# Kernel tuning notes

Measured on AMD Instinct MI355X. Metric: run time of the kernel, lower is better.

Reference implementation:

```python
import jax, jax.numpy as jnp
import numpy as np

EPS = 1e-5
SLOPE = 0.2
K = 20
BINS = [1, 2, 4, 8, 16, 32]


def knn(x_t, k):
    # x_t: (B, N, C) -> idx (B, N, k) of nearest neighbors (by L2, incl. self)
    xx = jnp.sum(x_t * x_t, axis=-1)  # (B, N)
    pd = 2.0 * jnp.einsum('bnc,bmc->bnm', x_t, x_t) - xx[:, :, None] - xx[:, None, :]
    _, idx = jax.lax.top_k(pd, k)
    return idx


def edge_features(x_t, idx):
    # x_t: (B, N, C), idx: (B, N, k) -> (B, N, k, 2C) = [nbr - ctr, ctr]
    B = x_t.shape[0]
    nbr = x_t[jnp.arange(B)[:, None, None], idx]          # (B, N, k, C) gather
    ctr = jnp.broadcast_to(x_t[:, :, None, :], nbr.shape)
    return jnp.concatenate([nbr - ctr, ctr], axis=-1)


def batchnorm(h, gamma, beta, axes):
    # training-mode BN: normalize with batch statistics over `axes` (channel last)
    m = jnp.mean(h, axis=axes, keepdims=True)
    v = jnp.var(h, axis=axes, keepdims=True)
    return (h - m) * jax.lax.rsqrt(v + EPS) * gamma + beta


def lrelu(h):
    return jnp.where(h >= 0, h, SLOPE * h)


def edgeconv(x_t, W, g, b):
    # 1x1 conv over edge features + BN + LeakyReLU + max over k neighbors
    e = edge_features(x_t, knn(x_t, K))            # (B, N, k, 2C)
    h = jnp.einsum('bnkc,oc->bnko', e, W)          # per-edge GEMM
    h = lrelu(batchnorm(h, g, b, (0, 1, 2)))
    return jnp.max(h, axis=2)                      # (B, N, Cout)


def setup_inputs() -> dict:
    key = jax.random.key(0)
    ks = jax.random.split(key, 8)
    B, N = 4, 2048
    d = {'x': jax.random.normal(ks[0], (B, 3, N), dtype=jnp.float32)}
    # conv weights (out, in); BN gamma=1, beta=0 as in torch init
    d['W1'] = jax.random.normal(ks[1], (64, 6), dtype=jnp.float32) * 0.1
    d['g1'] = jnp.ones((64,), jnp.float32); d['b1'] = jnp.zeros((64,), jnp.float32)
    d['W2'] = jax.random.normal(ks[2], (64, 128), dtype=jnp.float32) * 0.1
    d['g2'] = jnp.ones((64,), jnp.float32); d['b2'] = jnp.zeros((64,), jnp.float32)
    d['W3'] = jax.random.normal(ks[3], (128, 128), dtype=jnp.float32) * 0.1
    d['g3'] = jnp.ones((128,), jnp.float32); d['b3'] = jnp.zeros((128,), jnp.float32)
    d['W4'] = jax.random.normal(ks[4], (256, 256), dtype=jnp.float32) * 0.1
    d['g4'] = jnp.ones((256,), jnp.float32); d['b4'] = jnp.zeros((256,), jnp.float32)
    d['W5'] = jax.random.normal(ks[5], (1024, 512), dtype=jnp.float32) * 0.05
    d['g5'] = jnp.ones((1024,), jnp.float32); d['b5'] = jnp.zeros((1024,), jnp.float32)
    d['Wf'] = jax.random.normal(ks[6], (256, 1024), dtype=jnp.float32) * 0.03
    d['bfeat'] = jax.random.normal(ks[7], (256,), dtype=jnp.float32) * 0.01
    return d


def reference(x, W1, g1, b1, W2, g2, b2, W3, g3, b3, W4, g4, b4, W5, g5, b5, Wf, bfeat):
    B, _, N = x.shape
    x_t = jnp.transpose(x, (0, 2, 1))              # (B, N, 3)
    x1 = edgeconv(x_t, W1, g1, b1)                 # (B, N, 64)
    x2 = edgeconv(x1, W2, g2, b2)                  # (B, N, 64)
    x3 = edgeconv(x2, W3, g3, b3)                  # (B, N, 128)
    x4 = edgeconv(x3, W4, g4, b4)                  # (B, N, 256)
    xc = jnp.concatenate([x1, x2, x3, x4], axis=-1)  # (B, N, 512)
    h = jnp.einsum('bnc,oc->bno', xc, W5)          # (B, N, 1024)
    h = lrelu(batchnorm(h, g5, b5, (0, 1)))
    F = h.shape[-1]
    feats = []
    for nb in BINS:  # horizontal pyramid pooling over contiguous point chunks
        z = h.reshape(B, nb, N // nb, F)
        feats.append(jnp.max(z, axis=2) + jnp.mean(z, axis=2))
    bins = jnp.concatenate(feats, axis=1)          # (B, 63, F)
    out = jnp.einsum('bsf,of->sbo', bins, Wf) + bfeat  # (63, B, 256)
    return out
```

## Files before the change

kernel.cpp:

```cpp
#include <hip/hip_runtime.h>
#include <hip/hip_bf16.h>
#include <cstdint>
#include <cstddef>

#define B_SZ   4
#define N_PTS  2048
#define KNN    20
#define BN_ROWS (B_SZ * N_PTS)
#define EPSV   1e-5f
#define SLOPEV 0.2f

#define MODE_GD   0
#define MODE_DIST 1

typedef __attribute__((ext_vector_type(8))) short bf16x8;
typedef __attribute__((ext_vector_type(4))) float f32x4;

__global__ void k_transpose(const float* __restrict__ x, float* __restrict__ xt,
                            float* __restrict__ xx)
{
    int i = blockIdx.x * 256 + threadIdx.x;
    if (i >= BN_ROWS) return;
    int b = i >> 11, n = i & 2047;
    float v0 = x[((b * 3 + 0) << 11) + n];
    float v1 = x[((b * 3 + 1) << 11) + n];
    float v2 = x[((b * 3 + 2) << 11) + n];
    xt[i * 3 + 0] = v0; xt[i * 3 + 1] = v1; xt[i * 3 + 2] = v2;
    xx[i] = fmaf(v0, v0, fmaf(v1, v1, v2 * v2));
}

__global__ void k_prepw_all(const float* __restrict__ W1, const float* __restrict__ W2,
                            const float* __restrict__ W3, const float* __restrict__ W4,
                            const float* __restrict__ W5, const float* __restrict__ Wf,
                            float* __restrict__ wc, __hip_bfloat16* __restrict__ w5h,
                            float* __restrict__ wft)
{
    int i = blockIdx.x * 256 + threadIdx.x;
    if (i >= 876928) return;
    if (i >= 614784) {
        int e = i - 614784;
        int o = e >> 10, f = e & 1023;
        wft[f * 256 + o] = Wf[e];
        return;
    }
    if (i >= 90496) {
        int e = i - 90496;
        w5h[e] = __float2bfloat16(W5[e]);
        return;
    }
    const float* W; int O, C, off;
    if      (i < 384)   { W = W1; O = 64;  C = 3;   off = 0; }
    else if (i < 8576)  { W = W2; O = 64;  C = 64;  off = 384; }
    else if (i < 24960) { W = W3; O = 128; C = 64;  off = 8576; }
    else                { W = W4; O = 256; C = 128; off = 24960; }
    int e = i - off, j = e / C, c = e - j * C;
    float v;
    if (j < O) v = W[j * 2 * C + c];
    else { int jo = j - O; v = W[jo * 2 * C + C + c] - W[jo * 2 * C + c]; }
    wc[i] = v;
}

template<int MODE, bool VEC>
__launch_bounds__(256)
__global__ void k_mm128(const float* __restrict__ A, int lda,
                        const float* __restrict__ Bm, int ldb,
                        const float* __restrict__ xx, int b0,
                        float* __restrict__ C1, float* __restrict__ C2,
                        int Nn, int Kd)
{
    constexpr int LDA_ = 132;
    constexpr int LDB_ = (MODE == MODE_DIST) ? 132 : 68;
    constexpr int SMEMF = 32 * LDA_ + 32 * LDB_;
    __shared__ float smem[SMEMF];
    float* As = smem;
    float* Bs = smem + 32 * LDA_;
    float* T  = smem;
    const int tid = threadIdx.x;
    const int tx  = tid & 15;
    const int ty  = tid >> 4;

    int m0, n0;
    if constexpr (MODE == MODE_DIST) {
        int t = blockIdx.x;
        int it, jt;
        if (t < 120) {
            int i = 0;
            for (; i < 15; ++i) { int cnt = 15 - i; if (t < cnt) break; t -= cnt; }
            it = i; jt = i + 1 + t;
        } else {
            it = jt = t - 120;
        }
        m0 = it * 128;
        n0 = jt * 128;
    } else {
        m0 = blockIdx.y * 128;
        n0 = blockIdx.x * 64;
    }

    const float* Ab;
    const float* Bb;
    int ldbe;
    if constexpr (MODE == MODE_DIST) {
        const int b = b0 + blockIdx.z;
        Ab = A + (size_t)b * N_PTS * lda;
        Bb = Ab;
        ldbe = lda;
    } else {
        Ab = A; Bb = Bm; ldbe = ldb;
    }

    constexpr int NJH = (MODE == MODE_DIST) ? 2 : 1;
    float acc[2][NJH][4][4] = {};

    for (int k0 = 0; k0 < Kd; k0 += 32) {
        #pragma unroll
        for (int r = 0; r < 4; ++r) {
            int e = r * 256 + tid, row = e >> 3, kq = e & 7;
            if constexpr (VEC) {
                float4 v = *(const float4*)&Ab[(size_t)(m0 + row) * lda + k0 + kq * 4];
                As[(kq * 4 + 0) * LDA_ + row] = v.x;
                As[(kq * 4 + 1) * LDA_ + row] = v.y;
                As[(kq * 4 + 2) * LDA_ + row] = v.z;
                As[(kq * 4 + 3) * LDA_ + row] = v.w;
            } else {
                #pragma unroll
                for (int j = 0; j < 4; ++j) {
                    int kg = k0 + kq * 4 + j;
                    As[(kq * 4 + j) * LDA_ + row] =
                        (kg < Kd) ? Ab[(size_t)(m0 + row) * lda + kg] : 0.f;
                }
            }
        }
        constexpr int BR = (MODE == MODE_DIST) ? 4 : 2;
        #pragma unroll
        for (int r = 0; r < BR; ++r) {
            int e = r * 256 + tid, row = e >> 3, kq = e & 7;
            if constexpr (VEC) {
                float4 v = *(const float4*)&Bb[(size_t)(n0 + row) * ldbe + k0 + kq * 4];
                Bs[(kq * 4 + 0) * LDB_ + row] = v.x;
                Bs[(kq * 4 + 1) * LDB_ + row] = v.y;
                Bs[(kq * 4 + 2) * LDB_ + row] = v.z;
                Bs[(kq * 4 + 3) * LDB_ + row] = v.w;
            } else {
                #pragma unroll
                for (int j = 0; j < 4; ++j) {
                    int kg = k0 + kq * 4 + j;
                    Bs[(kq * 4 + j) * LDB_ + row] =
                        (kg < Kd) ? Bb[(size_t)(n0 + row) * ldbe + kg] : 0.f;
                }
            }
        }
        __syncthreads();

        int klen = Kd - k0; if (klen > 32) klen = 32;
        #pragma unroll 8
        for (int kk = 0; kk < klen; ++kk) {
            float4 a0 = *(const float4*)&As[kk * LDA_ + ty * 4];
            float4 a1 = *(const float4*)&As[kk * LDA_ + 64 + ty * 4];
            float av[2][4] = {{a0.x,a0.y,a0.z,a0.w},{a1.x,a1.y,a1.z,a1.w}};
            if constexpr (MODE == MODE_DIST) {
                float4 b0q = *(const float4*)&Bs[kk * LDB_ + tx * 4];
                float4 b1q = *(const float4*)&Bs[kk * LDB_ + 64 + tx * 4];
                float bw[2][4] = {{b0q.x,b0q.y,b0q.z,b0q.w},{b1q.x,b1q.y,b1q.z,b1q.w}};
                #pragma unroll
                for (int ih = 0; ih < 2; ++ih)
                    #pragma unroll
                    for (int jh = 0; jh < 2; ++jh)
                        #pragma unroll
                        for (int ii = 0; ii < 4; ++ii)
                            #pragma unroll
                            for (int jj = 0; jj < 4; ++jj)
                                acc[ih][jh][ii][jj] = fmaf(av[ih][ii], bw[jh][jj], acc[ih][jh][ii][jj]);
            } else {
                float4 bq = *(const float4*)&Bs[kk * LDB_ + tx * 4];
                float bw[4] = {bq.x, bq.y, bq.z, bq.w};
                #pragma unroll
                for (int ih = 0; ih < 2; ++ih)
                    #pragma unroll
                    for (int ii = 0; ii < 4; ++ii)
                        #pragma unroll
                        for (int jj = 0; jj < 4; ++jj)
                            acc[ih][0][ii][jj] = fmaf(av[ih][ii], bw[jj], acc[ih][0][ii][jj]);
            }
        }
        __syncthreads();
    }

    if constexpr (MODE == MODE_DIST) {
        const float* xxb = xx + (b0 + blockIdx.z) * N_PTS;
        float xj[2][4];
        #pragma unroll
        for (int jh = 0; jh < 2; ++jh) {
            float4 v = *(const float4*)&xxb[n0 + jh * 64 + tx * 4];
            xj[jh][0] = v.x; xj[jh][1] = v.y; xj[jh][2] = v.z; xj[jh][3] = v.w;
        }
        float xiv[2][4];
        #pragma unroll
        for (int ih = 0; ih < 2; ++ih)
            #pragma unroll
            for (int i = 0; i < 4; ++i)
                xiv[ih][i] = xxb[m0 + ih * 64 + ty * 4 + i];
        const bool diag = (m0 == n0);
        const size_t zoff = (size_t)blockIdx.z * N_PTS;

        #pragma unroll
        for (int ih = 0; ih < 2; ++ih)
            #pragma unroll
            for (int i = 0; i < 4; ++i) {
                int gi = m0 + ih * 64 + ty * 4 + i;
                float xi = xiv[ih][i];
                size_t base = (zoff + gi) * N_PTS;
                #pragma unroll
                for (int jh = 0; jh < 2; ++jh) {
                    int gj = n0 + jh * 64 + tx * 4;
                    float4 v;
                    v.x = 2.f * acc[ih][jh][i][0] - xi - xj[jh][0];
                    v.y = 2.f * acc[ih][jh][i][1] - xi - xj[jh][1];
                    v.z = 2.f * acc[ih][jh][i][2] - xi - xj[jh][2];
                    v.w = 2.f * acc[ih][jh][i][3] - xi - xj[jh][3];
                    if (diag) {
                        if (gi == gj + 0) v.x = 0.f;
                        if (gi == gj + 1) v.y = 0.f;
                        if (gi == gj + 2) v.z = 0.f;
                        if (gi == gj + 3) v.w = 0.f;
                    }
                    *(float4*)&C1[base + gj] = v;
                }
            }

        if (!diag) {
            #pragma unroll
            for (int jh = 0; jh < 2; ++jh) {
                #pragma unroll
                for (int c = 0; c < 4; ++c) {
                    float xjc = xj[jh][c];
                    #pragma unroll
                    for (int ih = 0; ih < 2; ++ih) {
                        float4 tv;
                        tv.x = 2.f * acc[ih][jh][0][c] - xjc - xiv[ih][0];
                        tv.y = 2.f * acc[ih][jh][1][c] - xjc - xiv[ih][1];
                        tv.z = 2.f * acc[ih][jh][2][c] - xjc - xiv[ih][2];
                        tv.w = 2.f * acc[ih][jh][3][c] - xjc - xiv[ih][3];
                        *(float4*)&T[(tx * 4 + c) * LDA_ + ih * 64 + ty * 4] = tv;
                    }
                }
                __syncthreads();
                #pragma unroll
                for (int r = 0; r < 8; ++r) {
                    int e = r * 256 + tid;
                    int jr = e >> 5, c4 = e & 31;
                    float4 tv = *(const float4*)&T[jr * LDA_ + c4 * 4];
                    *(float4*)&C1[(zoff + n0 + jh * 64 + jr) * N_PTS + m0 + c4 * 4] = tv;
                }
                __syncthreads();
            }
        }
    } else {
        const int Oo = Nn >> 1;
        #pragma unroll
        for (int ih = 0; ih < 2; ++ih)
            #pragma unroll
            for (int i = 0; i < 4; ++i) {
                int row = m0 + ih * 64 + ty * 4 + i;
                int colg = n0 + tx * 4;
                float4 v = make_float4(acc[ih][0][i][0], acc[ih][0][i][1],
                                       acc[ih][0][i][2], acc[ih][0][i][3]);
                if (colg < Oo) *(float4*)&C1[(size_t)row * Oo + colg] = v;
                else           *(float4*)&C2[(size_t)row * Oo + colg - Oo] = v;
            }
    }
}

__launch_bounds__(256)
__global__ void k_gemm5(const unsigned short* __restrict__ Ah,
                        const unsigned short* __restrict__ Bh,
                        float* __restrict__ Cf,
                        float* __restrict__ ssum, float* __restrict__ ssumsq)
{
    constexpr int LDA = 72;
    __shared__ unsigned short As[128 * LDA];
    __shared__ unsigned short Bs[128 * LDA];
    const int tid  = threadIdx.x;
    const int lane = tid & 63;
    const int w    = tid >> 6;
    const int wr   = w >> 1, wcl = w & 1;
    const int quad = lane >> 4;
    const int l16  = lane & 15;
    const int m0 = blockIdx.y * 128;
    const int n0 = blockIdx.x * 128;

    f32x4 acc[4][4] = {};

    for (int k0 = 0; k0 < 512; k0 += 64) {
        #pragma unroll
        for (int r = 0; r < 4; ++r) {
            int e = r * 256 + tid, row = e >> 3, kq = e & 7;
            *(uint4*)&As[row * LDA + kq * 8] =
                *(const uint4*)&Ah[(size_t)(m0 + row) * 512 + k0 + kq * 8];
        }
        #pragma unroll
        for (int r = 0; r < 4; ++r) {
            int e = r * 256 + tid, row = e >> 3, kq = e & 7;
            *(uint4*)&Bs[row * LDA + kq * 8] =
                *(const uint4*)&Bh[(size_t)(n0 + row) * 512 + k0 + kq * 8];
        }
        __syncthreads();
        #pragma unroll
        for (int kk = 0; kk < 64; kk += 32) {
            bf16x8 af[4], bfr[4];
            #pragma unroll
            for (int i = 0; i < 4; ++i)
                af[i] = *(const bf16x8*)&As[(wr * 64 + i * 16 + l16) * LDA + kk + quad * 8];
            #pragma unroll
            for (int j = 0; j < 4; ++j)
                bfr[j] = *(const bf16x8*)&Bs[(wcl * 64 + j * 16 + l16) * LDA + kk + quad * 8];
            #pragma unroll
            for (int i = 0; i < 4; ++i)
                #pragma unroll
                for (int j = 0; j < 4; ++j)
                    acc[i][j] = __builtin_amdgcn_mfma_f32_16x16x32_bf16(af[i], bfr[j], acc[i][j], 0, 0, 0);
        }
        __syncthreads();
    }

    #pragma unroll
    for (int i = 0; i < 4; ++i) {
        int rbase = m0 + wr * 64 + i * 16 + quad * 4;
        #pragma unroll
        for (int j = 0; j < 4; ++j) {
            int col = n0 + wcl * 64 + j * 16 + l16;
            #pragma unroll
            for (int r = 0; r < 4; ++r)
                Cf[(size_t)(rbase + r) * 1024 + col] = acc[i][j][r];
        }
    }

    float* sredS = (float*)As;
    float* sredQ = (float*)Bs;
    #pragma unroll
    for (int j = 0; j < 4; ++j) {
        float s = 0.f, q = 0.f;
        #pragma unroll
        for (int i = 0; i < 4; ++i)
            #pragma unroll
            for (int r = 0; r < 4; ++r) {
                float v = acc[i][j][r];
                s += v; q = fmaf(v, v, q);
            }
        int coll = wcl * 64 + j * 16 + l16;
        int slot = wr * 4 + quad;
        sredS[coll * 8 + slot] = s;
        sredQ[coll * 8 + slot] = q;
    }
    __syncthreads();
    if (tid < 128) {
        float s = 0.f, q = 0.f;
        #pragma unroll
        for (int t = 0; t < 8; ++t) { s += sredS[tid * 8 + t]; q += sredQ[tid * 8 + t]; }
        ssum  [blockIdx.y * 1024 + n0 + tid] = s;
        ssumsq[blockIdx.y * 1024 + n0 + tid] = q;
    }
}

__launch_bounds__(256)
__global__ void k_select(const float* __restrict__ D2, int* __restrict__ idx_out)
{
    const int lane = threadIdx.x & 63;
    const int w    = threadIdx.x >> 6;
    const int qloc = blockIdx.x * 4 + w;
    const float* row = D2 + (size_t)qloc * N_PTS;

    unsigned key[32];
    #pragma unroll
    for (int c = 0; c < 8; ++c) {
        float4 v = *(const float4*)&row[c * 256 + lane * 4];
        float vv[4] = {v.x, v.y, v.z, v.w};
        #pragma unroll
        for (int r = 0; r < 4; ++r) {
            unsigned u = __float_as_uint(vv[r]);
            key[c * 4 + r] = ((int)u >= 0) ? (u | 0x80000000u) : ~u;
        }
    }

    unsigned lo = 0u, hi = 0xFFFFFFFFu;
    while (lo < hi) {
        unsigned mid = lo + ((hi - lo) >> 1);
        int cnt = 0;
        #pragma unroll
        for (int e = 0; e < 32; ++e)
            cnt += __popcll(__ballot(key[e] > mid));
        if (cnt < KNN) hi = mid; else lo = mid + 1;
    }
    const unsigned T = lo;

    int* outp = idx_out + (size_t)qloc * KNN;
    const unsigned long long ltmask = (lane == 0) ? 0ull : (~0ull >> (64 - lane));
    int base = 0;
    #pragma unroll
    for (int e = 0; e < 32; ++e) {
        bool p = key[e] > T;
        unsigned long long m = __ballot(p);
        if (p) {
            int pos = base + __popcll(m & ltmask);
            outp[pos] = (e >> 2) * 256 + lane * 4 + (e & 3);
        }
        base += __popcll(m);
    }
    #pragma unroll
    for (int e = 0; e < 32; ++e) {
        bool p = key[e] == T;
        unsigned long long m = __ballot(p);
        if (p) {
            int pos = base + __popcll(m & ltmask);
            if (pos < KNN) outp[pos] = (e >> 2) * 256 + lane * 4 + (e & 3);
        }
        base += __popcll(m);
    }
}

template<int O, int NSEQ>
__launch_bounds__(256)
__global__ void k_gather(const float* __restrict__ gtab, const float* __restrict__ dtab,
                         const int* __restrict__ idx,
                         float* __restrict__ hmax, float* __restrict__ hmin,
                         float* __restrict__ ssum, float* __restrict__ ssumsq)
{
    constexpr int NPB = 256 / O;
    const int grp = threadIdx.x / O;
    const int o   = threadIdx.x & (O - 1);
    float accS = 0.f, accS2 = 0.f;
    const int rowsPerBlock = NPB * NSEQ;
    const int batch = blockIdx.x & 3;
    const int chunk = blockIdx.x >> 2;
    const int bbase = batch << 11;
    for (int s = 0; s < NSEQ; ++s) {
        int row = bbase + chunk * rowsPerBlock + s * NPB + grp;
        const int* ip = idx + (size_t)row * KNN;
        float gmax = -INFINITY, gmin = INFINITY, gs = 0.f, gs2 = 0.f;
        for (int k = 0; k < KNN; ++k) {
            int nb = ip[k];
            float v = gtab[(size_t)(bbase + nb) * O + o];
            gmax = fmaxf(gmax, v);
            gmin = fminf(gmin, v);
            gs  += v;
            gs2  = fmaf(v, v, gs2);
        }
        float d = dtab[(size_t)row * O + o];
        hmax[(size_t)row * O + o] = gmax + d;
        hmin[(size_t)row * O + o] = gmin + d;
        accS  += gs + (float)KNN * d;
        accS2 += gs2 + 2.f * d * gs + (float)KNN * d * d;
    }
    int bank = blockIdx.x & 63;
    atomicAdd(&ssum[bank * O + o], accS);
    atomicAdd(&ssumsq[bank * O + o], accS2);
}

template<int O, bool WRITE_XX>
__launch_bounds__(256)
__global__ void k_normalize(const float* __restrict__ hmax, const float* __restrict__ hmin,
                            const float* __restrict__ ssum, const float* __restrict__ ssumsq,
                            const float* __restrict__ gamma, const float* __restrict__ beta,
                            float invM, float* __restrict__ xcs,
                            __hip_bfloat16* __restrict__ xch, float* __restrict__ xx)
{
    const int tid = threadIdx.x;
    const int o   = tid & (O - 1);
    float s = 0.f, s2 = 0.f;
    #pragma unroll 8
    for (int bk = 0; bk < 64; ++bk) { s += ssum[bk * O + o]; s2 += ssumsq[bk * O + o]; }
    float mean = s * invM;
    float var  = fmaf(-mean, mean, s2 * invM);
    float sc   = gamma[o] * rsqrtf(var + EPSV);
    float sh   = beta[o] - mean * sc;

    constexpr int R = 256 / O;
    const int rloc = tid / O;
    __shared__ float part[4];
    const int ngroups = BN_ROWS / R;
    for (int gidx = blockIdx.x; gidx < ngroups; gidx += gridDim.x) {
        int row = gidx * R + rloc;
        size_t i = (size_t)row * O + o;
        float h = (sc >= 0.f) ? hmax[i] : hmin[i];
        float y = fmaf(h, sc, sh);
        y = (y >= 0.f) ? y : SLOPEV * y;
        xcs[(size_t)row * 512 + o] = y;
        xch[(size_t)row * 512 + o] = __float2bfloat16(y);
        if constexpr (WRITE_XX) {
            float p = y * y;
            #pragma unroll
            for (int sft = 32; sft >= 1; sft >>= 1) p += __shfl_xor(p, sft, 64);
            if constexpr (O == 64) {
                if ((tid & 63) == 0) xx[row] = p;
            } else {
                if ((tid & 63) == 0) part[tid >> 6] = p;
                __syncthreads();
                if constexpr (O == 128) {
                    if (tid < 2) xx[gidx * R + tid] = part[2 * tid] + part[2 * tid + 1];
                } else {
                    if (tid == 0) xx[gidx * R] = (part[0] + part[1]) + (part[2] + part[3]);
                }
                __syncthreads();
            }
        }
    }
}

__global__ void k_seg(const float* __restrict__ h,
                      const float* __restrict__ ssum, const float* __restrict__ ssumsq,
                      const float* __restrict__ gamma, const float* __restrict__ beta,
                      float* __restrict__ smax, float* __restrict__ ssumseg)
{
    int f = blockIdx.y * 256 + threadIdx.x;
    float s = 0.f, s2 = 0.f;
    #pragma unroll 8
    for (int bk = 0; bk < 64; ++bk) { s += ssum[bk * 1024 + f]; s2 += ssumsq[bk * 1024 + f]; }
    const float invM = 1.f / (float)BN_ROWS;
    float mean = s * invM;
    float var  = fmaf(-mean, mean, s2 * invM);
    float sc   = gamma[f] * rsqrtf(var + EPSV);
    float sh   = beta[f] - mean * sc;

    int seg = blockIdx.x;
    float mx = -INFINITY, sm = 0.f;
    int n0 = seg * 64;
    for (int i = 0; i < 64; ++i) {
        float v = fmaf(h[(size_t)(n0 + i) * 1024 + f], sc, sh);
        v = (v >= 0.f) ? v : SLOPEV * v;
        mx = fmaxf(mx, v); sm += v;
    }
    smax[(size_t)seg * 1024 + f]    = mx;
    ssumseg[(size_t)seg * 1024 + f] = sm;
}

__launch_bounds__(256)
__global__ void k_final(const float* __restrict__ smax, const float* __restrict__ ssg,
                        const float* __restrict__ Wft, const float* __restrict__ bfeat,
                        float* __restrict__ out)
{
    __shared__ float row[1024];
    __shared__ float part[1024];
    const int tid = threadIdx.x;
    int sb = blockIdx.x;
    int s = sb >> 2, b = sb & 3;
    int nb = (s == 0) ? 1 : (s < 3) ? 2 : (s < 7) ? 4 : (s < 15) ? 8 : (s < 31) ? 16 : 32;
    int idxL = s - (nb - 1);
    int segc = 32 / nb;
    int seg0 = b * 32 + idxL * segc;
    float inv = 1.f / (float)(64 * segc);
    for (int c = tid; c < 1024; c += 256) {
        float mx = -INFINITY, sm = 0.f;
        for (int t = 0; t < segc; ++t) {
            mx = fmaxf(mx, smax[(size_t)(seg0 + t) * 1024 + c]);
            sm += ssg[(size_t)(seg0 + t) * 1024 + c];
        }
        row[c] = mx + sm * inv;
    }
    __syncthreads();

    const int lane = tid & 63;
    const int w    = tid >> 6;
    const float* rw = row + w * 256;
    const float* wp = Wft + (size_t)(w * 256) * 256 + lane * 4;
    float4 a0 = {0,0,0,0}, a1 = {0,0,0,0}, a2 = {0,0,0,0}, a3 = {0,0,0,0};
    for (int f = 0; f < 256; f += 4) {
        float r0 = rw[f + 0], r1 = rw[f + 1], r2 = rw[f + 2], r3 = rw[f + 3];
        float4 w0 = *(const float4*)&wp[(size_t)(f + 0) * 256];
        float4 w1 = *(const float4*)&wp[(size_t)(f + 1) * 256];
        float4 w2 = *(const float4*)&wp[(size_t)(f + 2) * 256];
        float4 w3 = *(const float4*)&wp[(size_t)(f + 3) * 256];
        a0.x = fmaf(r0, w0.x, a0.x); a0.y = fmaf(r0, w0.y, a0.y);
        a0.z = fmaf(r0, w0.z, a0.z); a0.w = fmaf(r0, w0.w, a0.w);
        a1.x = fmaf(r1, w1.x, a1.x); a1.y = fmaf(r1, w1.y, a1.y);
        a1.z = fmaf(r1, w1.z, a1.z); a1.w = fmaf(r1, w1.w, a1.w);
        a2.x = fmaf(r2, w2.x, a2.x); a2.y = fmaf(r2, w2.y, a2.y);
        a2.z = fmaf(r2, w2.z, a2.z); a2.w = fmaf(r2, w2.w, a2.w);
        a3.x = fmaf(r3, w3.x, a3.x); a3.y = fmaf(r3, w3.y, a3.y);
        a3.z = fmaf(r3, w3.z, a3.z); a3.w = fmaf(r3, w3.w, a3.w);
    }
    float4 a;
    a.x = (a0.x + a1.x) + (a2.x + a3.x);
    a.y = (a0.y + a1.y) + (a2.y + a3.y);
    a.z = (a0.z + a1.z) + (a2.z + a3.z);
    a.w = (a0.w + a1.w) + (a2.w + a3.w);
    *(float4*)&part[w * 256 + lane * 4] = a;
    __syncthreads();
    int o = tid;
    float acc = (part[o] + part[256 + o]) + (part[512 + o] + part[768 + o]);
    out[(size_t)sb * 256 + o] = acc + bfeat[o];
}

extern "C" void kernel_launch(void* const* d_in, const int* in_sizes, int n_in,
                              void* d_out, int out_size, void* d_ws, size_t ws_size,
                              hipStream_t stream)
{
    const float* x  = (const float*)d_in[0];
    const float* W1 = (const float*)d_in[1];
    const float* g1 = (const float*)d_in[2];
    const float* b1 = (const float*)d_in[3];
    const float* W2 = (const float*)d_in[4];
    const float* g2 = (const float*)d_in[5];
    const float* b2 = (const float*)d_in[6];
    const float* W3 = (const float*)d_in[7];
    const float* g3 = (const float*)d_in[8];
    const float* b3 = (const float*)d_in[9];
    const float* W4 = (const float*)d_in[10];
    const float* g4 = (const float*)d_in[11];
    const float* b4 = (const float*)d_in[12];
    const float* W5 = (const float*)d_in[13];
    const float* g5 = (const float*)d_in[14];
    const float* b5 = (const float*)d_in[15];
    const float* Wf = (const float*)d_in[16];
    const float* bfeat = (const float*)d_in[17];
    float* out = (float*)d_out;
    float* ws  = (float*)d_ws;

    float* xt1   = ws + 0;
    int*   idx   = (int*)(ws + 24576);
    float* xx    = ws + 188416;
    float* xc    = ws + 196608;
    float* hmax  = ws + 4390912;
    float* hmin  = ws + 6488064;
    float* stats = ws + 8585216;
    float* smax  = ws + 8650752;
    float* ssg   = ws + 8781824;
    float* wc    = ws + 8912896;
    float* big   = ws + 9003520;
    float* gtab  = big;
    float* dtab  = big + 2097152;
    __hip_bfloat16* xch = (__hip_bfloat16*)(ws + 25780736);
    __hip_bfloat16* w5h = (__hip_bfloat16*)(ws + 27877888);
    float* wft   = ws + 28140032;
    float* l5s   = ws + 28402176;
    float* l5q   = ws + 28467712;

    hipMemsetAsync(stats, 0, 65536 * sizeof(float), stream);
    k_transpose<<<32, 256, 0, stream>>>(x, xt1, xx);
    k_prepw_all<<<3426, 256, 0, stream>>>(W1, W2, W3, W4, W5, Wf, wc, w5h, wft);

    const float invMk = 1.f / (float)(BN_ROWS * KNN);

    {
        float* ss = stats + 0;
        k_mm128<MODE_DIST, false><<<dim3(136, 1, 4), 256, 0, stream>>>(xt1, 3, nullptr, 0, xx, 0, big, nullptr, N_PTS, 3);
        k_select<<<2048, 256, 0, stream>>>(big, idx);
        k_mm128<MODE_GD, false><<<dim3(2, 64, 1), 256, 0, stream>>>(xt1, 3, wc, 3, nullptr, 0, gtab, dtab, 128, 3);
        k_gather<64, 8><<<256, 256, 0, stream>>>(gtab, dtab, idx, hmax, hmin, ss, ss + 4096);
        k_normalize<64, true><<<512, 256, 0, stream>>>(hmax, hmin, ss, ss + 4096, g1, b1, invMk, xc + 0, xch + 0, xx);
    }
    {
        float* ss = stats + 8192;
        k_mm128<MODE_DIST, true><<<dim3(136, 1, 4), 256, 0, stream>>>(xc + 0, 512, nullptr, 0, xx, 0, big, nullptr, N_PTS, 64);
        k_select<<<2048, 256, 0, stream>>>(big, idx);
        k_mm128<MODE_GD, true><<<dim3(2, 64, 1), 256, 0, stream>>>(xc + 0, 512, wc + 384, 64, nullptr, 0, gtab, dtab, 128, 64);
        k_gather<64, 8><<<256, 256, 0, stream>>>(gtab, dtab, idx, hmax, hmin, ss, ss + 4096);
        k_normalize<64, true><<<512, 256, 0, stream>>>(hmax, hmin, ss, ss + 4096, g2, b2, invMk, xc + 64, xch + 64, xx);
    }
    {
        float* ss = stats + 16384;
        k_mm128<MODE_DIST, true><<<dim3(136, 1, 4), 256, 0, stream>>>(xc + 64, 512, nullptr, 0, xx, 0, big, nullptr, N_PTS, 64);
        k_select<<<2048, 256, 0, stream>>>(big, idx);
        k_mm128<MODE_GD, true><<<dim3(4, 64, 1), 256, 0, stream>>>(xc + 64, 512, wc + 8576, 64, nullptr, 0, gtab, dtab, 256, 64);
        k_gather<128, 8><<<512, 256, 0, stream>>>(gtab, dtab, idx, hmax, hmin, ss, ss + 8192);
        k_normalize<128, true><<<512, 256, 0, stream>>>(hmax, hmin, ss, ss + 8192, g3, b3, invMk, xc + 128, xch + 128, xx);
    }
    {
        float* ss = stats + 32768;
        k_mm128<MODE_DIST, true><<<dim3(136, 1, 4), 256, 0, stream>>>(xc + 128, 512, nullptr, 0, xx, 0, big, nullptr, N_PTS, 128);
        k_select<<<2048, 256, 0, stream>>>(big, idx);
        k_mm128<MODE_GD, true><<<dim3(8, 64, 1), 256, 0, stream>>>(xc + 128, 512, wc + 24960, 128, nullptr, 0, gtab, dtab, 512, 128);
        k_gather<256, 8><<<1024, 256, 0, stream>>>(gtab, dtab, idx, hmax, hmin, ss, ss + 16384);
        k_normalize<256, false><<<512, 256, 0, stream>>>(hmax, hmin, ss, ss + 16384, g4, b4, invMk, xc + 256, xch + 256, xx);
    }
    {
        k_gemm5<<<dim3(8, 64), 256, 0, stream>>>((const unsigned short*)xch, (const unsigned short*)w5h, big, l5s, l5q);
        k_seg<<<dim3(128, 4), 256, 0, stream>>>(big, l5s, l5q, g5, b5, smax, ssg);
        k_final<<<252, 256, 0, stream>>>(smax, ssg, wft, bfeat, out);
    }
}
```

Measured before the change: 577.1 us.

## Split distance GEMM tiles into 128x64 items with atomic work-queue scheduling

Replaces the 256-thread 128x128 pairwise-distance tile kernel with a 128-thread 128x64 variant. Tiles are claimed through an atomic ticket counter instead of blockIdx, giving 1088 smaller work items that balance better across CUs. The symmetric mirror write is restructured per 64-column half. The GD weight GEMM path also moves to 128 threads. The cost is smaller blocks with lower per-thread reuse, plus an extra atomic and barrier per tile.

Result: slower. 700.7 us (+21.4%).

```diff
diff --git a/kernel.cpp b/kernel.cpp
--- a/kernel.cpp
+++ b/kernel.cpp
@@ -61,107 +61,105 @@
 }
 
 template<int MODE, bool VEC>
-__launch_bounds__(256)
-__global__ void k_mm128(const float* __restrict__ A, int lda,
-                        const float* __restrict__ Bm, int ldb,
-                        const float* __restrict__ xx, int b0,
-                        float* __restrict__ C1, float* __restrict__ C2,
-                        int Nn, int Kd)
+__launch_bounds__(128)
+__global__ void k_mm64(const float* __restrict__ A, int lda,
+                       const float* __restrict__ Bm, int ldb,
+                       const float* __restrict__ xx, int* __restrict__ tick,
+                       float* __restrict__ C1, float* __restrict__ C2,
+                       int Nn, int Kd)
 {
     constexpr int LDA_ = 132;
-    constexpr int LDB_ = (MODE == MODE_DIST) ? 132 : 68;
-    constexpr int SMEMF = 32 * LDA_ + 32 * LDB_;
-    __shared__ float smem[SMEMF];
+    constexpr int LDB_ = 68;
+    __shared__ float smem[32 * LDA_ + 32 * LDB_];
+    __shared__ int s_t;
     float* As = smem;
     float* Bs = smem + 32 * LDA_;
     float* T  = smem;
     const int tid = threadIdx.x;
-    const int tx  = tid & 15;
-    const int ty  = tid >> 4;
-
-    int m0, n0;
-    if constexpr (MODE == MODE_DIST) {
-        int t = blockIdx.x;
-        int it, jt;
-        if (t < 120) {
-            int i = 0;
-            for (; i < 15; ++i) { int cnt = 15 - i; if (t < cnt) break; t -= cnt; }
-            it = i; jt = i + 1 + t;
+    const int tx  = tid & 7;
+    const int ty  = tid >> 3;
+
+    for (;;) {
+        int m0, n0, bz = 0;
+        bool diagitem = false, mirror = false;
+        if constexpr (MODE == MODE_DIST) {
+            if (tid == 0) s_t = atomicAdd(tick, 1);
+            __syncthreads();
+            const int t = s_t;
+            if (t >= 1088) return;
+            bz = t & 3;
+            int u = t >> 2;
+            int it, jt, half;
+            if (u < 240) {
+                int p = u >> 1; half = u & 1; mirror = true;
+                int i = 0;
+                for (; i < 15; ++i) { int cnt = 15 - i; if (p < cnt) break; p -= cnt; }
+                it = i; jt = i + 1 + p;
+            } else {
+                int d = u - 240; it = jt = d >> 1; half = d & 1; diagitem = true;
+            }
+            m0 = it * 128;
+            n0 = jt * 128 + half * 64;
         } else {
-            it = jt = t - 120;
-        }
-        m0 = it * 128;
-        n0 = jt * 128;
-    } else {
-        m0 = blockIdx.y * 128;
-        n0 = blockIdx.x * 64;
-    }
-
-    const float* Ab;
-    const float* Bb;
-    int ldbe;
-    if constexpr (MODE == MODE_DIST) {
-        const int b = b0 + blockIdx.z;
-        Ab = A + (size_t)b * N_PTS * lda;
-        Bb = Ab;
-        ldbe = lda;
-    } else {
-        Ab = A; Bb = Bm; ldbe = ldb;
-    }
-
-    constexpr int NJH = (MODE == MODE_DIST) ? 2 : 1;
-    float acc[2][NJH][4][4] = {};
-
-    for (int k0 = 0; k0 < Kd; k0 += 32) {
-        #pragma unroll
-        for (int r = 0; r < 4; ++r) {
-            int e = r * 256 + tid, row = e >> 3, kq = e & 7;
-            if constexpr (VEC) {
-                float4 v = *(const float4*)&Ab[(size_t)(m0 + row) * lda + k0 + kq * 4];
-                As[(kq * 4 + 0) * LDA_ + row] = v.x;
-                As[(kq * 4 + 1) * LDA_ + row] = v.y;
-                As[(kq * 4 + 2) * LDA_ + row] = v.z;
-                As[(kq * 4 + 3) * LDA_ + row] = v.w;
-            } else {
-                #pragma unroll
-                for (int j = 0; j < 4; ++j) {
-                    int kg = k0 + kq * 4 + j;
-                    As[(kq * 4 + j) * LDA_ + row] =
-                        (kg < Kd) ? Ab[(size_t)(m0 + row) * lda + kg] : 0.f;
+            m0 = blockIdx.y * 128;
+            n0 = blockIdx.x * 64;
+        }
+
+        const float* Ab; const float* Bb; int ldbe;
+        if constexpr (MODE == MODE_DIST) {
+            Ab = A + (size_t)bz * N_PTS * lda;  Bb = Ab;  ldbe = lda;
+        } else { Ab = A; Bb = Bm; ldbe = ldb; }
+
+        float acc[2][2][4][4] = {};
+
+        for (int k0 = 0; k0 < Kd; k0 += 32) {
+            #pragma unroll
+            for (int r = 0; r < 8; ++r) {
+                int e = r * 128 + tid, row = e >> 3, kq = e & 7;
+                if constexpr (VEC) {
+                    float4 v = *(const float4*)&Ab[(size_t)(m0 + row) * lda + k0 + kq * 4];
+                    As[(kq * 4 + 0) * LDA_ + row] = v.x;
+                    As[(kq * 4 + 1) * LDA_ + row] = v.y;
+                    As[(kq * 4 + 2) * LDA_ + row] = v.z;
+                    As[(kq * 4 + 3) * LDA_ + row] = v.w;
+                } else {
+                    #pragma unroll
+                    for (int j = 0; j < 4; ++j) {
+                        int kg = k0 + kq * 4 + j;
+                        As[(kq * 4 + j) * LDA_ + row] =
+                            (kg < Kd) ? Ab[(size_t)(m0 + row) * lda + kg] : 0.f;
+                    }
                 }
             }
-        }
-        constexpr int BR = (MODE == MODE_DIST) ? 4 : 2;
-        #pragma unroll
-        for (int r = 0; r < BR; ++r) {
-            int e = r * 256 + tid, row = e >> 3, kq = e & 7;
-            if constexpr (VEC) {
-                float4 v = *(const float4*)&Bb[(size_t)(n0 + row) * ldbe + k0 + kq * 4];
-                Bs[(kq * 4 + 0) * LDB_ + row] = v.x;
-                Bs[(kq * 4 + 1) * LDB_ + row] = v.y;
-                Bs[(kq * 4 + 2) * LDB_ + row] = v.z;
-                Bs[(kq * 4 + 3) * LDB_ + row] = v.w;
-            } else {
-                #pragma unroll
-                for (int j = 0; j < 4; ++j) {
-                    int kg = k0 + kq * 4 + j;
-                    Bs[(kq * 4 + j) * LDB_ + row] =
-                        (kg < Kd) ? Bb[(size_t)(n0 + row) * ldbe + kg] : 0.f;
+            #pragma unroll
+            for (int r = 0; r < 4; ++r) {
+                int e = r * 128 + tid, row = e >> 3, kq = e & 7;
+                if constexpr (VEC) {
+                    float4 v = *(const float4*)&Bb[(size_t)(n0 + row) * ldbe + k0 + kq * 4];
+                    Bs[(kq * 4 + 0) * LDB_ + row] = v.x;
+                    Bs[(kq * 4 + 1) * LDB_ + row] = v.y;
+                    Bs[(kq * 4 + 2) * LDB_ + row] = v.z;
+                    Bs[(kq * 4 + 3) * LDB_ + row] = v.w;
+                } else {
+                    #pragma unroll
+                    for (int j = 0; j < 4; ++j) {
+                        int kg = k0 + kq * 4 + j;
+                        Bs[(kq * 4 + j) * LDB_ + row] =
+                            (kg < Kd) ? Bb[(size_t)(n0 + row) * ldbe + kg] : 0.f;
+                    }
                 }
             }
-        }
-        __syncthreads();
-
-        int klen = Kd - k0; if (klen > 32) klen = 32;
-        #pragma unroll 8
-        for (int kk = 0; kk < klen; ++kk) {
-            float4 a0 = *(const float4*)&As[kk * LDA_ + ty * 4];
-            float4 a1 = *(const float4*)&As[kk * LDA_ + 64 + ty * 4];
-            float av[2][4] = {{a0.x,a0.y,a0.z,a0.w},{a1.x,a1.y,a1.z,a1.w}};
-            if constexpr (MODE == MODE_DIST) {
-                float4 b0q = *(const float4*)&Bs[kk * LDB_ + tx * 4];
-                float4 b1q = *(const float4*)&Bs[kk * LDB_ + 64 + tx * 4];
-                float bw[2][4] = {{b0q.x,b0q.y,b0q.z,b0q.w},{b1q.x,b1q.y,b1q.z,b1q.w}};
+            __syncthreads();
+
+            int klen = Kd - k0; if (klen > 32) klen = 32;
+            #pragma unroll 8
+            for (int kk = 0; kk < klen; ++kk) {
+                float4 a0 = *(const float4*)&As[kk * LDA_ + ty * 4];
+                float4 a1 = *(const float4*)&As[kk * LDA_ + 64 + ty * 4];
+                float4 b0 = *(const float4*)&Bs[kk * LDB_ + tx * 4];
+                float4 b1 = *(const float4*)&Bs[kk * LDB_ + 32 + tx * 4];
+                float av[2][4] = {{a0.x,a0.y,a0.z,a0.w},{a1.x,a1.y,a1.z,a1.w}};
+                float bw[2][4] = {{b0.x,b0.y,b0.z,b0.w},{b1.x,b1.y,b1.z,b1.w}};
                 #pragma unroll
                 for (int ih = 0; ih < 2; ++ih)
                     #pragma unroll
@@ -171,103 +169,95 @@
                             #pragma unroll
                             for (int jj = 0; jj < 4; ++jj)
                                 acc[ih][jh][ii][jj] = fmaf(av[ih][ii], bw[jh][jj], acc[ih][jh][ii][jj]);
-            } else {
-                float4 bq = *(const float4*)&Bs[kk * LDB_ + tx * 4];
-                float bw[4] = {bq.x, bq.y, bq.z, bq.w};
+            }
+            __syncthreads();
+        }
+
+        if constexpr (MODE == MODE_DIST) {
+            const float* xxb = xx + bz * N_PTS;
+            float xj[2][4];
+            #pragma unroll
+            for (int jh = 0; jh < 2; ++jh) {
+                float4 v = *(const float4*)&xxb[n0 + jh * 32 + tx * 4];
+                xj[jh][0] = v.x; xj[jh][1] = v.y; xj[jh][2] = v.z; xj[jh][3] = v.w;
+            }
+            float xiv[2][4];
+            #pragma unroll
+            for (int ih = 0; ih < 2; ++ih)
                 #pragma unroll
-                for (int ih = 0; ih < 2; ++ih)
+                for (int i = 0; i < 4; ++i)
+                    xiv[ih][i] = xxb[m0 + ih * 64 + ty * 4 + i];
+            const size_t zoff = (size_t)bz * N_PTS;
+
+            #pragma unroll
+            for (int ih = 0; ih < 2; ++ih)
+                #pragma unroll
+                for (int i = 0; i < 4; ++i) {
+                    int gi = m0 + ih * 64 + ty * 4 + i;
+                    float xi = xiv[ih][i];
+                    size_t base = (zoff + gi) * (size_t)N_PTS;
                     #pragma unroll
-                    for (int ii = 0; ii < 4; ++ii)
-                        #pragma unroll
-                        for (int jj = 0; jj < 4; ++jj)
-                            acc[ih][0][ii][jj] = fmaf(av[ih][ii], bw[jj], acc[ih][0][ii][jj]);
-            }
-        }
-        __syncthreads();
-    }
-
-    if constexpr (MODE == MODE_DIST) {
-        const float* xxb = xx + (b0 + blockIdx.z) * N_PTS;
-        float xj[2][4];
-        #pragma unroll
-        for (int jh = 0; jh < 2; ++jh) {
-            float4 v = *(const float4*)&xxb[n0 + jh * 64 + tx * 4];
-            xj[jh][0] = v.x; xj[jh][1] = v.y; xj[jh][2] = v.z; xj[jh][3] = v.w;
-        }
-        float xiv[2][4];
-        #pragma unroll
-        for (int ih = 0; ih < 2; ++ih)
-            #pragma unroll
-            for (int i = 0; i < 4; ++i)
-                xiv[ih][i] = xxb[m0 + ih * 64 + ty * 4 + i];
-        const bool diag = (m0 == n0);
-        const size_t zoff = (size_t)blockIdx.z * N_PTS;
-
-        #pragma unroll
-        for (int ih = 0; ih < 2; ++ih)
-            #pragma unroll
-            for (int i = 0; i < 4; ++i) {
-                int gi = m0 + ih * 64 + ty * 4 + i;
-                float xi = xiv[ih][i];
-                size_t base = (zoff + gi) * N_PTS;
-                #pragma unroll
-                for (int jh = 0; jh < 2; ++jh) {
-                    int gj = n0 + jh * 64 + tx * 4;
-                    float4 v;
-                    v.x = 2.f * acc[ih][jh][i][0] - xi - xj[jh][0];
-                    v.y = 2.f * acc[ih][jh][i][1] - xi - xj[jh][1];
-                    v.z = 2.f * acc[ih][jh][i][2] - xi - xj[jh][2];
-                    v.w = 2.f * acc[ih][jh][i][3] - xi - xj[jh][3];
-                    if (diag) {
-                        if (gi == gj + 0) v.x = 0.f;
-                        if (gi == gj + 1) v.y = 0.f;
-                        if (gi == gj + 2) v.z = 0.f;
-                        if (gi == gj + 3) v.w = 0.f;
-                    }
-                    *(float4*)&C1[base + gj] = v;
-                }
-            }
-
-        if (!diag) {
-            #pragma unroll
-            for (int jh = 0; jh < 2; ++jh) {
-                #pragma unroll
-                for (int c = 0; c < 4; ++c) {
-                    float xjc = xj[jh][c];
-                    #pragma unroll
-                    for (int ih = 0; ih < 2; ++ih) {
-                        float4 tv;
-                        tv.x = 2.f * acc[ih][jh][0][c] - xjc - xiv[ih][0];
-                        tv.y = 2.f * acc[ih][jh][1][c] - xjc - xiv[ih][1];
-                        tv.z = 2.f * acc[ih][jh][2][c] - xjc - xiv[ih][2];
-                        tv.w = 2.f * acc[ih][jh][3][c] - xjc - xiv[ih][3];
-                        *(float4*)&T[(tx * 4 + c) * LDA_ + ih * 64 + ty * 4] = tv;
+                    for (int jh = 0; jh < 2; ++jh) {
+                        int gj = n0 + jh * 32 + tx * 4;
+                        float4 v;
+                        v.x = 2.f * acc[ih][jh][i][0] - xi - xj[jh][0];
+                        v.y = 2.f * acc[ih][jh][i][1] - xi - xj[jh][1];
+                        v.z = 2.f * acc[ih][jh][i][2] - xi - xj[jh][2];
+                        v.w = 2.f * acc[ih][jh][i][3] - xi - xj[jh][3];
+                        if (diagitem) {
+                            if (gi == gj + 0) v.x = 0.f;
+                            if (gi == gj + 1) v.y = 0.f;
+                            if (gi == gj + 2) v.z = 0.f;
+                            if (gi == gj + 3) v.w = 0.f;
+                        }
+                        *(float4*)&C1[base + gj] = v;
                     }
                 }
-                __syncthreads();
+
+            if (mirror) {
                 #pragma unroll
-                for (int r = 0; r < 8; ++r) {
-                    int e = r * 256 + tid;
-                    int jr = e >> 5, c4 = e & 31;
-                    float4 tv = *(const float4*)&T[jr * LDA_ + c4 * 4];
-                    *(float4*)&C1[(zoff + n0 + jh * 64 + jr) * N_PTS + m0 + c4 * 4] = tv;
+                for (int mh = 0; mh < 2; ++mh) {
+                    #pragma unroll
+                    for (int jh = 0; jh < 2; ++jh)
+                        #pragma unroll
+                        for (int j = 0; j < 4; ++j) {
+                            float xjc = xj[jh][j];
+                            float4 tv;
+                            tv.x = 2.f * acc[mh][jh][0][j] - xjc - xiv[mh][0];
+                            tv.y = 2.f * acc[mh][jh][1][j] - xjc - xiv[mh][1];
+                            tv.z = 2.f * acc[mh][jh][2][j] - xjc - xiv[mh][2];
+                            tv.w = 2.f * acc[mh][jh][3][j] - xjc - xiv[mh][3];
+                            *(float4*)&T[(jh * 32 + tx * 4 + j) * LDB_ + ty * 4] = tv;
+                        }
+                    __syncthreads();
+                    #pragma unroll
+                    for (int r = 0; r < 8; ++r) {
+                        int e = r * 128 + tid;
+                        int jr = e >> 4, c4 = e & 15;
+                        float4 tv = *(const float4*)&T[jr * LDB_ + c4 * 4];
+                        *(float4*)&C1[(zoff + n0 + jr) * (size_t)N_PTS + m0 + mh * 64 + c4 * 4] = tv;
+                    }
+                    __syncthreads();
                 }
-                __syncthreads();
-            }
-        }
-    } else {
-        const int Oo = Nn >> 1;
-        #pragma unroll
-        for (int ih = 0; ih < 2; ++ih)
-            #pragma unroll
-            for (int i = 0; i < 4; ++i) {
-                int row = m0 + ih * 64 + ty * 4 + i;
-                int colg = n0 + tx * 4;
-                float4 v = make_float4(acc[ih][0][i][0], acc[ih][0][i][1],
-                                       acc[ih][0][i][2], acc[ih][0][i][3]);
-                if (colg < Oo) *(float4*)&C1[(size_t)row * Oo + colg] = v;
-                else           *(float4*)&C2[(size_t)row * Oo + colg - Oo] = v;
-            }
+            }
+        } else {
+            const int Oo = Nn >> 1;
+            float* Cd; int nb2;
+            if (n0 < Oo) { Cd = C1; nb2 = n0; } else { Cd = C2; nb2 = n0 - Oo; }
+            #pragma unroll
+            for (int ih = 0; ih < 2; ++ih)
+                #pragma unroll
+                for (int i = 0; i < 4; ++i) {
+                    int row = m0 + ih * 64 + ty * 4 + i;
+                    #pragma unroll
+                    for (int jh = 0; jh < 2; ++jh) {
+                        float4 v = make_float4(acc[ih][jh][i][0], acc[ih][jh][i][1],
+                                               acc[ih][jh][i][2], acc[ih][jh][i][3]);
+                        *(float4*)&Cd[(size_t)row * Oo + nb2 + jh * 32 + tx * 4] = v;
+                    }
+                }
+            return;
+        }
     }
 }
 
@@ -633,8 +623,10 @@
     float* wft   = ws + 28140032;
     float* l5s   = ws + 28402176;
     float* l5q   = ws + 28467712;
+    int*   tick  = (int*)(ws + 28533248);
 
     hipMemsetAsync(stats, 0, 65536 * sizeof(float), stream);
+    hipMemsetAsync(tick, 0, 16 * sizeof(int), stream);
     k_transpose<<<32, 256, 0, stream>>>(x, xt1, xx);
     k_prepw_all<<<3426, 256, 0, stream>>>(W1, W2, W3, W4, W5, Wf, wc, w5h, wft);
 
@@ -642,33 +634,33 @@
 
     {
         float* ss = stats + 0;
-        k_mm128<MODE_DIST, false><<<dim3(136, 1, 4), 256, 0, stream>>>(xt1, 3, nullptr, 0, xx, 0, big, nullptr, N_PTS, 3);
+        k_mm64<MODE_DIST, false><<<1088, 128, 0, stream>>>(xt1, 3, nullptr, 0, xx, tick + 0, big, nullptr, N_PTS, 3);
         k_select<<<2048, 256, 0, stream>>>(big, idx);
-        k_mm128<MODE_GD, false><<<dim3(2, 64, 1), 256, 0, stream>>>(xt1, 3, wc, 3, nullptr, 0, gtab, dtab, 128, 3);
+        k_mm64<MODE_GD, false><<<dim3(2, 64, 1), 128, 0, stream>>>(xt1, 3, wc, 3, nullptr, nullptr, gtab, dtab, 128, 3);
         k_gather<64, 8><<<256, 256, 0, stream>>>(gtab, dtab, idx, hmax, hmin, ss, ss + 4096);
         k_normalize<64, true><<<512, 256, 0, stream>>>(hmax, hmin, ss, ss + 4096, g1, b1, invMk, xc + 0, xch + 0, xx);
     }
     {
         float* ss = stats + 8192;
-        k_mm128<MODE_DIST, true><<<dim3(136, 1, 4), 256, 0, stream>>>(xc + 0, 512, nullptr, 0, xx, 0, big, nullptr, N_PTS, 64);
+        k_mm64<MODE_DIST, true><<<1088, 128, 0, stream>>>(xc + 0, 512, nullptr, 0, xx, tick + 1, big, nullptr, N_PTS, 64);
         k_select<<<2048, 256, 0, stream>>>(big, idx);
-        k_mm128<MODE_GD, true><<<dim3(2, 64, 1), 256, 0, stream>>>(xc + 0, 512, wc + 384, 64, nullptr, 0, gtab, dtab, 128, 64);
+        k_mm64<MODE_GD, true><<<dim3(2, 64, 1), 128, 0, stream>>>(xc + 0, 512, wc + 384, 64, nullptr, nullptr, gtab, dtab, 128, 64);
         k_gather<64, 8><<<256, 256, 0, stream>>>(gtab, dtab, idx, hmax, hmin, ss, ss + 4096);
         k_normalize<64, true><<<512, 256, 0, stream>>>(hmax, hmin, ss, ss + 4096, g2, b2, invMk, xc + 64, xch + 64, xx);
     }
     {
         float* ss = stats + 16384;
-        k_mm128<MODE_DIST, true><<<dim3(136, 1, 4), 256, 0, stream>>>(xc + 64, 512, nullptr, 0, xx, 0, big, nullptr, N_PTS, 64);
+        k_mm64<MODE_DIST, true><<<1088, 128, 0, stream>>>(xc + 64, 512, nullptr, 0, xx, tick + 2, big, nullptr, N_PTS, 64);
         k_select<<<2048, 256, 0, stream>>>(big, idx);
-        k_mm128<MODE_GD, true><<<dim3(4, 64, 1), 256, 0, stream>>>(xc + 64, 512, wc + 8576, 64, nullptr, 0, gtab, dtab, 256, 64);
+        k_mm64<MODE_GD, true><<<dim3(4, 64, 1), 128, 0, stream>>>(xc + 64, 512, wc + 8576, 64, nullptr, nullptr, gtab, dtab, 256, 64);
         k_gather<128, 8><<<512, 256, 0, stream>>>(gtab, dtab, idx, hmax, hmin, ss, ss + 8192);
         k_normalize<128, true><<<512, 256, 0, stream>>>(hmax, hmin, ss, ss + 8192, g3, b3, invMk, xc + 128, xch + 128, xx);
     }
     {
         float* ss = stats + 32768;
-        k_mm128<MODE_DIST, true><<<dim3(136, 1, 4), 256, 0, stream>>>(xc + 128, 512, nullptr, 0, xx, 0, big, nullptr, N_PTS, 128);
+        k_mm64<MODE_DIST, true><<<1088, 128, 0, stream>>>(xc + 128, 512, nullptr, 0, xx, tick + 3, big, nullptr, N_PTS, 128);
         k_select<<<2048, 256, 0, stream>>>(big, idx);
-        k_mm128<MODE_GD, true><<<dim3(8, 64, 1), 256, 0, stream>>>(xc + 128, 512, wc + 24960, 128, nullptr, 0, gtab, dtab, 512, 128);
+        k_mm64<MODE_GD, true><<<dim3(8, 64, 1), 128, 0, stream>>>(xc + 128, 512, wc + 24960, 128, nullptr, nullptr, gtab, dtab, 512, 128);
         k_gather<256, 8><<<1024, 256, 0, stream>>>(gtab, dtab, idx, hmax, hmin, ss, ss + 16384);
         k_normalize<256, false><<<512, 256, 0, stream>>>(hmax, hmin, ss, ss + 16384, g4, b4, invMk, xc + 256, xch + 256, xx);
     }
```

## Prefetch next global tile into registers and double-buffer LDS reads in k_mm128

Applied to the files above, without the earlier changes.

For the vectorized path of the FP32 tiled GEMM kernel, the next K-slab of A and B is loaded from global memory into registers while the current slab is being computed. Inside the slab, the next row of shared-memory operands is loaded ahead of the FMAs, and the inner loop is fully unrolled to 32. Launch bounds now request 2 blocks per CU. The aim is to hide global and LDS latency behind compute, at the cost of more registers, which could cut occupancy or cause spills under the tighter launch bound.

After: 618.4 us. 7.1% more time.

```diff
diff --git a/kernel.cpp b/kernel.cpp
--- a/kernel.cpp
+++ b/kernel.cpp
@@ -61,7 +61,7 @@
 }
 
 template<int MODE, bool VEC>
-__launch_bounds__(256)
+__launch_bounds__(256, 2)
 __global__ void k_mm128(const float* __restrict__ A, int lda,
                         const float* __restrict__ Bm, int ldb,
                         const float* __restrict__ xx, int b0,
@@ -70,6 +70,7 @@
 {
     constexpr int LDA_ = 132;
     constexpr int LDB_ = (MODE == MODE_DIST) ? 132 : 68;
+    constexpr int BR   = (MODE == MODE_DIST) ? 4 : 2;
     constexpr int SMEMF = 32 * LDA_ + 32 * LDB_;
     __shared__ float smem[SMEMF];
     float* As = smem;
@@ -112,17 +113,88 @@
     constexpr int NJH = (MODE == MODE_DIST) ? 2 : 1;
     float acc[2][NJH][4][4] = {};
 
-    for (int k0 = 0; k0 < Kd; k0 += 32) {
-        #pragma unroll
-        for (int r = 0; r < 4; ++r) {
-            int e = r * 256 + tid, row = e >> 3, kq = e & 7;
-            if constexpr (VEC) {
-                float4 v = *(const float4*)&Ab[(size_t)(m0 + row) * lda + k0 + kq * 4];
-                As[(kq * 4 + 0) * LDA_ + row] = v.x;
-                As[(kq * 4 + 1) * LDA_ + row] = v.y;
-                As[(kq * 4 + 2) * LDA_ + row] = v.z;
-                As[(kq * 4 + 3) * LDA_ + row] = v.w;
-            } else {
+    if constexpr (VEC) {
+        float4 aR[4], bR[BR];
+        auto loadg = [&](int k0g) {
+            #pragma unroll
+            for (int r = 0; r < 4; ++r) {
+                int e = r * 256 + tid, row = e >> 3, kq = e & 7;
+                aR[r] = *(const float4*)&Ab[(size_t)(m0 + row) * lda + k0g + kq * 4];
+            }
+            #pragma unroll
+            for (int r = 0; r < BR; ++r) {
+                int e = r * 256 + tid, row = e >> 3, kq = e & 7;
+                bR[r] = *(const float4*)&Bb[(size_t)(n0 + row) * ldbe + k0g + kq * 4];
+            }
+        };
+        loadg(0);
+        for (int k0 = 0; k0 < Kd; k0 += 32) {
+            #pragma unroll
+            for (int r = 0; r < 4; ++r) {
+                int e = r * 256 + tid, row = e >> 3, kq = e & 7;
+                As[(kq * 4 + 0) * LDA_ + row] = aR[r].x;
+                As[(kq * 4 + 1) * LDA_ + row] = aR[r].y;
+                As[(kq * 4 + 2) * LDA_ + row] = aR[r].z;
+                As[(kq * 4 + 3) * LDA_ + row] = aR[r].w;
+            }
+            #pragma unroll
+            for (int r = 0; r < BR; ++r) {
+                int e = r * 256 + tid, row = e >> 3, kq = e & 7;
+                Bs[(kq * 4 + 0) * LDB_ + row] = bR[r].x;
+                Bs[(kq * 4 + 1) * LDB_ + row] = bR[r].y;
+                Bs[(kq * 4 + 2) * LDB_ + row] = bR[r].z;
+                Bs[(kq * 4 + 3) * LDB_ + row] = bR[r].w;
+            }
+            if (k0 + 32 < Kd) loadg(k0 + 32);
+            __syncthreads();
+
+            float4 ca0 = *(const float4*)&As[ty * 4];
+            float4 ca1 = *(const float4*)&As[64 + ty * 4];
+            float4 cb0 = *(const float4*)&Bs[tx * 4];
+            float4 cb1 = {};
+            if constexpr (MODE == MODE_DIST) cb1 = *(const float4*)&Bs[64 + tx * 4];
+            #pragma unroll
+            for (int kk = 0; kk < 32; ++kk) {
+                float4 na0 = ca0, na1 = ca1, nb0 = cb0, nb1 = cb1;
+                if (kk < 31) {
+                    na0 = *(const float4*)&As[(kk + 1) * LDA_ + ty * 4];
+                    na1 = *(const float4*)&As[(kk + 1) * LDA_ + 64 + ty * 4];
+                    nb0 = *(const float4*)&Bs[(kk + 1) * LDB_ + tx * 4];
+                    if constexpr (MODE == MODE_DIST)
+                        nb1 = *(const float4*)&Bs[(kk + 1) * LDB_ + 64 + tx * 4];
+                }
+                float av[2][4] = {{ca0.x,ca0.y,ca0.z,ca0.w},{ca1.x,ca1.y,ca1.z,ca1.w}};
+                if constexpr (MODE == MODE_DIST) {
+                    float bw[2][4] = {{cb0.x,cb0.y,cb0.z,cb0.w},{cb1.x,cb1.y,cb1.z,cb1.w}};
+                    #pragma unroll
+                    for (int ih = 0; ih < 2; ++ih)
+                        #pragma unroll
+                        for (int jh = 0; jh < 2; ++jh)
+                            #pragma unroll
+                            for (int ii = 0; ii < 4; ++ii)
+                                #pragma unroll
+                                for (int jj = 0; jj < 4; ++jj)
+                                    acc[ih][jh][ii][jj] = fmaf(av[ih][ii], bw[jh][jj], acc[ih][jh][ii][jj]);
+                } else {
+                    float bw[4] = {cb0.x, cb0.y, cb0.z, cb0.w};
+                    #pragma unroll
+                    for (int ih = 0; ih < 2; ++ih)
+                        #pragma unroll
+                        for (int ii = 0; ii < 4; ++ii)
+                            #pragma unroll
+                            for (int jj = 0; jj < 4; ++jj)
+                                acc[ih][0][ii][jj] = fmaf(av[ih][ii], bw[jj], acc[ih][0][ii][jj]);
+                }
+                ca0 = na0; ca1 = na1; cb0 = nb0;
+                if constexpr (MODE == MODE_DIST) cb1 = nb1;
+            }
+            __syncthreads();
+        }
+    } else {
+        for (int k0 = 0; k0 < Kd; k0 += 32) {
+            #pragma unroll
+            for (int r = 0; r < 4; ++r) {
+                int e = r * 256 + tid, row = e >> 3, kq = e & 7;
                 #pragma unroll
                 for (int j = 0; j < 4; ++j) {
                     int kg = k0 + kq * 4 + j;
@@ -130,18 +202,9 @@
                         (kg < Kd) ? Ab[(size_t)(m0 + row) * lda + kg] : 0.f;
                 }
             }
-        }
-        constexpr int BR = (MODE == MODE_DIST) ? 4 : 2;
-        #pragma unroll
-        for (int r = 0; r < BR; ++r) {
-            int e = r * 256 + tid, row = e >> 3, kq = e & 7;
-            if constexpr (VEC) {
-                float4 v = *(const float4*)&Bb[(size_t)(n0 + row) * ldbe + k0 + kq * 4];
-                Bs[(kq * 4 + 0) * LDB_ + row] = v.x;
-                Bs[(kq * 4 + 1) * LDB_ + row] = v.y;
-                Bs[(kq * 4 + 2) * LDB_ + row] = v.z;
-                Bs[(kq * 4 + 3) * LDB_ + row] = v.w;
-            } else {
+            #pragma unroll
+            for (int r = 0; r < BR; ++r) {
+                int e = r * 256 + tid, row = e >> 3, kq = e & 7;
                 #pragma unroll
                 for (int j = 0; j < 4; ++j) {
                     int kg = k0 + kq * 4 + j;
@@ -149,41 +212,41 @@
                         (kg < Kd) ? Bb[(size_t)(n0 + row) * ldbe + kg] : 0.f;
                 }
             }
-        }
-        __syncthreads();
-
-        int klen = Kd - k0; if (klen > 32) klen = 32;
-        #pragma unroll 8
-        for (int kk = 0; kk < klen; ++kk) {
-            float4 a0 = *(const float4*)&As[kk * LDA_ + ty * 4];
-            float4 a1 = *(const float4*)&As[kk * LDA_ + 64 + ty * 4];
-            float av[2][4] = {{a0.x,a0.y,a0.z,a0.w},{a1.x,a1.y,a1.z,a1.w}};
-            if constexpr (MODE == MODE_DIST) {
-                float4 b0q = *(const float4*)&Bs[kk * LDB_ + tx * 4];
-                float4 b1q = *(const float4*)&Bs[kk * LDB_ + 64 + tx * 4];
-                float bw[2][4] = {{b0q.x,b0q.y,b0q.z,b0q.w},{b1q.x,b1q.y,b1q.z,b1q.w}};
-                #pragma unroll
-                for (int ih = 0; ih < 2; ++ih)
+            __syncthreads();
+
+            int klen = Kd - k0; if (klen > 32) klen = 32;
+            #pragma unroll 8
+            for (int kk = 0; kk < klen; ++kk) {
+                float4 a0 = *(const float4*)&As[kk * LDA_ + ty * 4];
+                float4 a1 = *(const float4*)&As[kk * LDA_ + 64 + ty * 4];
+                float av[2][4] = {{a0.x,a0.y,a0.z,a0.w},{a1.x,a1.y,a1.z,a1.w}};
+                if constexpr (MODE == MODE_DIST) {
+                    float4 b0q = *(const float4*)&Bs[kk * LDB_ + tx * 4];
+                    float4 b1q = *(const float4*)&Bs[kk * LDB_ + 64 + tx * 4];
+                    float bw[2][4] = {{b0q.x,b0q.y,b0q.z,b0q.w},{b1q.x,b1q.y,b1q.z,b1q.w}};
                     #pragma unroll
-                    for (int jh = 0; jh < 2; ++jh)
+                    for (int ih = 0; ih < 2; ++ih)
+                        #pragma unroll
+                        for (int jh = 0; jh < 2; ++jh)
+                            #pragma unroll
+                            for (int ii = 0; ii < 4; ++ii)
+                                #pragma unroll
+                                for (int jj = 0; jj < 4; ++jj)
+                                    acc[ih][jh][ii][jj] = fmaf(av[ih][ii], bw[jh][jj], acc[ih][jh][ii][jj]);
+                } else {
+                    float4 bq = *(const float4*)&Bs[kk * LDB_ + tx * 4];
+                    float bw[4] = {bq.x, bq.y, bq.z, bq.w};
+                    #pragma unroll
+                    for (int ih = 0; ih < 2; ++ih)
                         #pragma unroll
                         for (int ii = 0; ii < 4; ++ii)
                             #pragma unroll
                             for (int jj = 0; jj < 4; ++jj)
-                                acc[ih][jh][ii][jj] = fmaf(av[ih][ii], bw[jh][jj], acc[ih][jh][ii][jj]);
-            } else {
-                float4 bq = *(const float4*)&Bs[kk * LDB_ + tx * 4];
-                float bw[4] = {bq.x, bq.y, bq.z, bq.w};
-                #pragma unroll
-                for (int ih = 0; ih < 2; ++ih)
-                    #pragma unroll
-                    for (int ii = 0; ii < 4; ++ii)
-                        #pragma unroll
-                        for (int jj = 0; jj < 4; ++jj)
-                            acc[ih][0][ii][jj] = fmaf(av[ih][ii], bw[jj], acc[ih][0][ii][jj]);
-            }
-        }
-        __syncthreads();
+                                acc[ih][0][ii][jj] = fmaf(av[ih][ii], bw[jj], acc[ih][0][ii][jj]);
+                }
+            }
+            __syncthreads();
+        }
     }
 
     if constexpr (MODE == MODE_DIST) {
```
